# Kernel optimization log

Measured on AMD Instinct MI355X. Metric: run time of the kernel, lower is better.

## Reference

```python
import jax, jax.numpy as jnp
import numpy as np

N = 200000   # n+m+p+q
EMB = 32
K = 3
NNZ = 3200000


def _spmm(vals, rows, cols, X):
    # sparse [N,N] @ dense [N,EMB] via gather + segment-sum scatter
    return jax.ops.segment_sum(vals[:, None] * X[cols], rows, num_segments=N)


def setup_inputs() -> dict:
    key = jax.random.key(0)
    k1, k2, k3, k4 = jax.random.split(key, 4)
    A_vals = jax.random.uniform(k1, (NNZ,), dtype=jnp.float32)
    W0 = jax.random.normal(k2, (N, EMB), dtype=jnp.float32) * 0.01
    alpha = jnp.ones((K + 1,), dtype=jnp.float32) / (K + 1)
    A_rows = jax.random.randint(k3, (NNZ,), 0, N, dtype=jnp.int32)
    A_cols = jax.random.randint(k4, (NNZ,), 0, N, dtype=jnp.int32)
    return {"A_vals": A_vals, "W0": W0, "alpha": alpha,
            "A_rows": A_rows, "A_cols": A_cols}


def reference(A_vals, W0, alpha, A_rows, A_cols):
    E = _spmm(A_vals, A_rows, A_cols, W0)  # E0 = A @ W0
    a = jax.nn.softmax(alpha)
    E_final = a[0] * E
    for i in range(K):  # k-hop propagation, weighted accumulation fused
        E = _spmm(A_vals, A_rows, A_cols, E)
        E_final = E_final + a[i + 1] * E
    return E_final
```

## Files before the change

### kernel.cpp

```cpp
#include <hip/hip_runtime.h>

#define EMB 32
#define BSHIFT 10
#define RPB 1024
#define NB 256
#define TILE 4096
#define PT_THREADS 256
#define PT_ITEMS 16
#define SP_THREADS 1024
#define COLMASK 0x3FFFF


__global__ void bucket_hist_kernel(const int* __restrict__ rows, int nnz,
                                   int* __restrict__ bhist, int nb) {
    __shared__ int h[NB];
    int t = threadIdx.x;
    h[t] = 0;
    __syncthreads();
    int stride = gridDim.x * blockDim.x;
    for (int i = blockIdx.x * blockDim.x + t; i < nnz; i += stride)
        atomicAdd(&h[rows[i] >> BSHIFT], 1);
    __syncthreads();
    if (t < nb && h[t] > 0) atomicAdd(&bhist[t], h[t]);
}

__global__ __launch_bounds__(PT_THREADS) void partition_kernel(
        const float* __restrict__ vals, const int* __restrict__ rows,
        const int* __restrict__ cols, int nnz,
        const int* __restrict__ bhist, int* __restrict__ cursor,
        int2* __restrict__ pairs_stage, unsigned short* __restrict__ lrow_stage) {
    __shared__ int locbase[NB];
    __shared__ int h[NB];
    __shared__ int sc[NB];
    __shared__ int delta[NB];
    __shared__ float s_val[TILE];
    __shared__ int s_pack[TILE];
    __shared__ unsigned short s_bkt[TILE];
    const int t = threadIdx.x;
    const int tile_start = blockIdx.x * TILE;
    const int tile_cnt = min(TILE, nnz - tile_start);

    const int ownb = bhist[t];
    locbase[t] = ownb;
    h[t] = 0;
    __syncthreads();
    for (int off = 1; off < NB; off <<= 1) {
        int add = (t >= off) ? locbase[t - off] : 0;
        __syncthreads();
        locbase[t] += add;
        __syncthreads();
    }
    const int eb = locbase[t] - ownb;

    float v[PT_ITEMS];
    int pk[PT_ITEMS], b[PT_ITEMS];
    #pragma unroll
    for (int k = 0; k < PT_ITEMS; ++k) {
        int i = tile_start + t + k * PT_THREADS;
        if (i < nnz) {
            int r = rows[i];
            v[k] = vals[i];
            pk[k] = cols[i] | ((r & (RPB - 1)) << 18);
            b[k] = r >> BSHIFT;
            atomicAdd(&h[b[k]], 1);
        } else {
            b[k] = -1;
        }
    }
    __syncthreads();
    const int own = h[t];
    sc[t] = own;
    __syncthreads();
    for (int off = 1; off < NB; off <<= 1) {
        int add = (t >= off) ? sc[t - off] : 0;
        __syncthreads();
        sc[t] += add;
        __syncthreads();
    }
    const int excl = sc[t] - own;
    if (own > 0) {
        int old = atomicAdd(&cursor[t], own);
        delta[t] = (eb + old) - excl;
    }
    h[t] = excl;
    __syncthreads();
    #pragma unroll
    for (int k = 0; k < PT_ITEMS; ++k) {
        if (b[k] >= 0) {
            int rank = atomicAdd(&h[b[k]], 1);
            s_val[rank] = v[k];
            s_pack[rank] = pk[k];
            s_bkt[rank] = (unsigned short)b[k];
        }
    }
    __syncthreads();
    for (int i = t; i < tile_cnt; i += PT_THREADS) {
        int bb = s_bkt[i];
        int gpos = delta[bb] + i;
        int pk_i = s_pack[i];
        pairs_stage[gpos] = make_int2(__float_as_int(s_val[i]), pk_i);
        lrow_stage[gpos] = (unsigned short)(((unsigned)pk_i) >> 18);
    }
}

__global__ __launch_bounds__(SP_THREADS) void bucket_sort_kernel(
        const int2* __restrict__ pairs_stage, const unsigned short* __restrict__ lrow_stage,
        const int* __restrict__ bhist, int n, int nnz,
        int* __restrict__ row_ptr, int2* __restrict__ pairs) {
    __shared__ int rh[RPB];
    __shared__ int rc[RPB];
    const int bkt = blockIdx.x;
    const int t = threadIdx.x;

    if (t < NB) rh[t] = bhist[t];
    __syncthreads();
    for (int off = 1; off < NB; off <<= 1) {
        int add = 0;
        if (t < NB && t >= off) add = rh[t - off];
        __syncthreads();
        if (t < NB) rh[t] += add;
        __syncthreads();
    }
    const int i0 = (bkt > 0) ? rh[bkt - 1] : 0;
    const int i1 = rh[bkt];
    __syncthreads();

    const int row0 = bkt << BSHIFT;
    const int nrows = min(RPB, n - row0);
    rh[t] = 0;
    __syncthreads();
    for (int i = i0 + t; i < i1; i += SP_THREADS)
        atomicAdd(&rh[lrow_stage[i]], 1);
    __syncthreads();
    const int own = rh[t];
    for (int off = 1; off < SP_THREADS; off <<= 1) {
        int add = (t >= off) ? rh[t - off] : 0;
        __syncthreads();
        rh[t] += add;
        __syncthreads();
    }
    const int excl = rh[t] - own;
    if (t < nrows) row_ptr[row0 + t] = i0 + excl;
    rc[t] = excl;
    if (bkt == 0 && t == 0) row_ptr[n] = nnz;
    __syncthreads();
    for (int i = i0 + t; i < i1; i += SP_THREADS) {
        int2 p = pairs_stage[i];
        int r = lrow_stage[i];
        int pos = i0 + atomicAdd(&rc[r], 1);
        pairs[pos] = make_int2(p.x, p.y & COLMASK);
    }
}


__global__ void softmax4_kernel(const float* __restrict__ alpha, float* __restrict__ coefs) {
    if (threadIdx.x == 0 && blockIdx.x == 0) {
        float m = fmaxf(fmaxf(alpha[0], alpha[1]), fmaxf(alpha[2], alpha[3]));
        float e0 = __expf(alpha[0] - m), e1 = __expf(alpha[1] - m);
        float e2 = __expf(alpha[2] - m), e3 = __expf(alpha[3] - m);
        float inv = 1.0f / (e0 + e1 + e2 + e3);
        coefs[0] = e0 * inv; coefs[1] = e1 * inv; coefs[2] = e2 * inv; coefs[3] = e3 * inv;
    }
}


template <bool INIT, bool STORE_E>
__global__ __launch_bounds__(256) void spmm_kernel(
        const int* __restrict__ row_ptr, const int2* __restrict__ pairs,
        const float* __restrict__ X, float* __restrict__ Eout,
        float* __restrict__ Efin, const float* __restrict__ coefs,
        int hop, int n) {
    int tid = blockIdx.x * blockDim.x + threadIdx.x;
    int row = tid >> 3;
    if (row >= n) return;
    const int sub = (tid & 7) * 4;
    int j = row_ptr[row];
    const int j1 = row_ptr[row + 1];
    float ax = 0.f, ay = 0.f, az = 0.f, aw = 0.f;

    if ((j & 1) && j < j1) {
        int2 p = pairs[j];
        float v = __int_as_float(p.x);
        const float4 x = *reinterpret_cast<const float4*>(X + (size_t)p.y * EMB + sub);
        ax = fmaf(v, x.x, ax); ay = fmaf(v, x.y, ay);
        az = fmaf(v, x.z, az); aw = fmaf(v, x.w, aw);
        ++j;
    }
    for (; j + 4 <= j1; j += 4) {
        const int4 pa = *reinterpret_cast<const int4*>(pairs + j);
        const int4 pb = *reinterpret_cast<const int4*>(pairs + j + 2);
        const float4 x0 = *reinterpret_cast<const float4*>(X + (size_t)pa.y * EMB + sub);
        const float4 x1 = *reinterpret_cast<const float4*>(X + (size_t)pa.w * EMB + sub);
        const float4 x2 = *reinterpret_cast<const float4*>(X + (size_t)pb.y * EMB + sub);
        const float4 x3 = *reinterpret_cast<const float4*>(X + (size_t)pb.w * EMB + sub);
        const float v0 = __int_as_float(pa.x), v1 = __int_as_float(pa.z);
        const float v2 = __int_as_float(pb.x), v3 = __int_as_float(pb.z);
        ax = fmaf(v0, x0.x, ax); ay = fmaf(v0, x0.y, ay);
        az = fmaf(v0, x0.z, az); aw = fmaf(v0, x0.w, aw);
        ax = fmaf(v1, x1.x, ax); ay = fmaf(v1, x1.y, ay);
        az = fmaf(v1, x1.z, az); aw = fmaf(v1, x1.w, aw);
        ax = fmaf(v2, x2.x, ax); ay = fmaf(v2, x2.y, ay);
        az = fmaf(v2, x2.z, az); aw = fmaf(v2, x2.w, aw);
        ax = fmaf(v3, x3.x, ax); ay = fmaf(v3, x3.y, ay);
        az = fmaf(v3, x3.z, az); aw = fmaf(v3, x3.w, aw);
    }
    for (; j < j1; ++j) {
        int2 p = pairs[j];
        float v = __int_as_float(p.x);
        const float4 x = *reinterpret_cast<const float4*>(X + (size_t)p.y * EMB + sub);
        ax = fmaf(v, x.x, ax); ay = fmaf(v, x.y, ay);
        az = fmaf(v, x.z, az); aw = fmaf(v, x.w, aw);
    }

    const size_t o = (size_t)row * EMB + sub;
    if (STORE_E)
        *reinterpret_cast<float4*>(Eout + o) = make_float4(ax, ay, az, aw);
    const float a = coefs[hop];
    if (INIT) {
        *reinterpret_cast<float4*>(Efin + o) = make_float4(a * ax, a * ay, a * az, a * aw);
    } else {
        float4 f = *reinterpret_cast<const float4*>(Efin + o);
        f.x += a * ax; f.y += a * ay; f.z += a * az; f.w += a * aw;
        *reinterpret_cast<float4*>(Efin + o) = f;
    }
}


__global__ void spmm_atomic_kernel(const float* __restrict__ vals, const int* __restrict__ rows,
                                   const int* __restrict__ cols, int nnz,
                                   const float* __restrict__ X, float* __restrict__ Eout) {
    long long stride = (long long)gridDim.x * blockDim.x;
    long long total = (long long)nnz * 8;
    for (long long t = (long long)blockIdx.x * blockDim.x + threadIdx.x; t < total; t += stride) {
        int i = (int)(t >> 3);
        int sub = ((int)t & 7) * 4;
        float v = vals[i];
        const float4 x = *reinterpret_cast<const float4*>(X + (long long)cols[i] * EMB + sub);
        float* o = Eout + (long long)rows[i] * EMB + sub;
        atomicAdd(o + 0, v * x.x);
        atomicAdd(o + 1, v * x.y);
        atomicAdd(o + 2, v * x.z);
        atomicAdd(o + 3, v * x.w);
    }
}

template <bool INIT>
__global__ void axpy_kernel(const float* __restrict__ E, float* __restrict__ Efin,
                            const float* __restrict__ coefs, int hop, int total4) {
    int i = blockIdx.x * blockDim.x + threadIdx.x;
    if (i >= total4) return;
    float a = coefs[hop];
    float4 e = reinterpret_cast<const float4*>(E)[i];
    if (INIT) {
        reinterpret_cast<float4*>(Efin)[i] = make_float4(a * e.x, a * e.y, a * e.z, a * e.w);
    } else {
        float4 f = reinterpret_cast<float4*>(Efin)[i];
        f.x += a * e.x; f.y += a * e.y; f.z += a * e.z; f.w += a * e.w;
        reinterpret_cast<float4*>(Efin)[i] = f;
    }
}


extern "C" void kernel_launch(void* const* d_in, const int* in_sizes, int n_in,
                              void* d_out, int out_size, void* d_ws, size_t ws_size,
                              hipStream_t stream) {
    const float* A_vals = (const float*)d_in[0];
    const float* W0     = (const float*)d_in[1];
    const float* alpha  = (const float*)d_in[2];
    const int*   A_rows = (const int*)d_in[3];
    const int*   A_cols = (const int*)d_in[4];
    const int nnz = in_sizes[0];
    const int n   = in_sizes[1] / EMB;
    float* Efin = (float*)d_out;

    char* ws = (char*)d_ws;
    size_t off = 0;
    auto alloc = [&](size_t bytes) -> void* {
        void* p = (void*)(ws + off);
        off += (bytes + 255) & ~(size_t)255;
        return p;
    };

    float* Ebuf0 = (float*)alloc((size_t)n * EMB * 4);
    float* Ebuf1 = (float*)alloc((size_t)n * EMB * 4);
    float* coefs = (float*)alloc(4 * sizeof(float));
    int*  row_ptr = (int*)alloc((size_t)(n + 1) * 4);
    int*  bhist   = (int*)alloc(NB * 4);
    int*  cursor  = (int*)alloc(NB * 4);
    int2* pairs   = (int2*)alloc((size_t)nnz * 8);
    size_t off_csr = off;

    int2* pairs_stage = (int2*)Ebuf0;
    unsigned short* lrow_stage = (unsigned short*)Ebuf1;

    const int nb = (n + RPB - 1) >> BSHIFT;
    const bool use_csr = (ws_size >= off_csr) && (nb <= NB) && (n <= COLMASK + 1) &&
                         ((size_t)nnz * 8 <= (size_t)n * EMB * 4);

    softmax4_kernel<<<1, 64, 0, stream>>>(alpha, coefs);

    if (use_csr) {
        hipMemsetAsync(bhist, 0, 2 * NB * 4, stream);
        bucket_hist_kernel<<<1024, 256, 0, stream>>>(A_rows, nnz, bhist, nb);
        partition_kernel<<<(nnz + TILE - 1) / TILE, PT_THREADS, 0, stream>>>(
            A_vals, A_rows, A_cols, nnz, bhist, cursor, pairs_stage, lrow_stage);
        bucket_sort_kernel<<<nb, SP_THREADS, 0, stream>>>(
            pairs_stage, lrow_stage, bhist, n, nnz, row_ptr, pairs);

        int blocks = (n * 8 + 255) / 256;
        spmm_kernel<true,  true ><<<blocks, 256, 0, stream>>>(row_ptr, pairs, W0,    Ebuf0, Efin, coefs, 0, n);
        spmm_kernel<false, true ><<<blocks, 256, 0, stream>>>(row_ptr, pairs, Ebuf0, Ebuf1, Efin, coefs, 1, n);
        spmm_kernel<false, true ><<<blocks, 256, 0, stream>>>(row_ptr, pairs, Ebuf1, Ebuf0, Efin, coefs, 2, n);
        spmm_kernel<false, false><<<blocks, 256, 0, stream>>>(row_ptr, pairs, Ebuf0, Ebuf1, Efin, coefs, 3, n);
    } else {
        const float* X = W0;
        float* bufs[2] = {Ebuf0, Ebuf1};
        int total4 = n * EMB / 4;
        int ablocks = (total4 + 255) / 256;
        for (int hop = 0; hop < 4; ++hop) {
            float* Eo = bufs[hop & 1];
            hipMemsetAsync(Eo, 0, (size_t)n * EMB * 4, stream);
            spmm_atomic_kernel<<<2048, 256, 0, stream>>>(A_vals, A_rows, A_cols, nnz, X, Eo);
            if (hop == 0)
                axpy_kernel<true ><<<ablocks, 256, 0, stream>>>(Eo, Efin, coefs, hop, total4);
            else
                axpy_kernel<false><<<ablocks, 256, 0, stream>>>(Eo, Efin, coefs, hop, total4);
            X = Eo;
        }
    }
}
```

Before: 471.7 us.

## Bin rows by length within buckets and process two rows per thread group

The bucket sort now groups rows inside each 1024-row bucket by nonzero count and permutes them into slots. It emits a slot-ordered row pointer plus an order map back to the original rows, so neighbouring 8-lane groups in a wavefront get rows of similar length. The SpMM kernel then has each 8-lane group handle two adjacent slots at once, interleaving their gathers to raise memory-level parallelism. The aim is less load imbalance and divergence within wavefronts when row lengths are random. The cost is an extra indirection for output rows, scattered row writes, more registers per thread, and added work in the sort kernel.

```diff
diff --git a/kernel.cpp b/kernel.cpp
--- a/kernel.cpp
+++ b/kernel.cpp
@@ -105,18 +105,22 @@
 
 __global__ __launch_bounds__(SP_THREADS) void bucket_sort_kernel(
         const int2* __restrict__ pairs_stage, const unsigned short* __restrict__ lrow_stage,
-        const int* __restrict__ bhist, int n, int nnz,
-        int* __restrict__ row_ptr, int2* __restrict__ pairs) {
+        const int* __restrict__ bhist, int n, int nnz, int nb,
+        int* __restrict__ rps, int* __restrict__ order, int2* __restrict__ pairs) {
     __shared__ int rh[RPB];
+    __shared__ int pre[RPB];
     __shared__ int rc[RPB];
+    __shared__ unsigned short srOf[RPB];
+    __shared__ unsigned short tOf[RPB];
+    __shared__ int binCnt[66];
+    __shared__ int binBase[66];
     const int bkt = blockIdx.x;
     const int t = threadIdx.x;
 
     if (t < NB) rh[t] = bhist[t];
     __syncthreads();
     for (int off = 1; off < NB; off <<= 1) {
-        int add = 0;
-        if (t < NB && t >= off) add = rh[t - off];
+        int add = (t < NB && t >= off) ? rh[t - off] : 0;
         __syncthreads();
         if (t < NB) rh[t] += add;
         __syncthreads();
@@ -128,26 +132,46 @@
     const int row0 = bkt << BSHIFT;
     const int nrows = min(RPB, n - row0);
     rh[t] = 0;
+    if (t < 66) binCnt[t] = 0;
     __syncthreads();
     for (int i = i0 + t; i < i1; i += SP_THREADS)
         atomicAdd(&rh[lrow_stage[i]], 1);
     __syncthreads();
     const int own = rh[t];
-    for (int off = 1; off < SP_THREADS; off <<= 1) {
-        int add = (t >= off) ? rh[t - off] : 0;
-        __syncthreads();
-        rh[t] += add;
-        __syncthreads();
-    }
-    const int excl = rh[t] - own;
-    if (t < nrows) row_ptr[row0 + t] = i0 + excl;
-    rc[t] = excl;
-    if (bkt == 0 && t == 0) row_ptr[n] = nnz;
+    const bool valid = t < nrows;
+    const int bin = valid ? min(own, 63) : 65 - 1;
+    const int rb = atomicAdd(&binCnt[bin], 1);
+    __syncthreads();
+    if (t == 0) {
+        int s = 0;
+        for (int k = 0; k < 65; ++k) { binBase[k] = s; s += binCnt[k]; }
+    }
+    __syncthreads();
+    const int sr = binBase[bin] + rb;
+    srOf[t] = (unsigned short)sr;
+    tOf[sr] = (unsigned short)t;
+    pre[sr] = valid ? own : 0;
+    __syncthreads();
+    for (int off = 1; off < RPB; off <<= 1) {
+        int add = (t >= off) ? pre[t - off] : 0;
+        __syncthreads();
+        pre[t] += add;
+        __syncthreads();
+    }
+    const int tt = tOf[t];
+    const int lenSlot = rh[tt];
+    const int startSlot = pre[t] - lenSlot;
+    const int gslot = (bkt << BSHIFT) + t;
+    rps[gslot] = i0 + startSlot;
+    order[gslot] = (tt < nrows) ? (row0 + tt) : -1;
+    if (bkt == nb - 1 && t == 0) rps[nb << BSHIFT] = nnz;
+    __syncthreads();
+    rc[t] = i0 + (pre[srOf[t]] - rh[t]);
     __syncthreads();
     for (int i = i0 + t; i < i1; i += SP_THREADS) {
         int2 p = pairs_stage[i];
         int r = lrow_stage[i];
-        int pos = i0 + atomicAdd(&rc[r], 1);
+        int pos = atomicAdd(&rc[r], 1);
         pairs[pos] = make_int2(p.x, p.y & COLMASK);
     }
 }
@@ -166,27 +190,34 @@
 
 template <bool INIT, bool STORE_E>
 __global__ __launch_bounds__(256) void spmm_kernel(
-        const int* __restrict__ row_ptr, const int2* __restrict__ pairs,
-        const float* __restrict__ X, float* __restrict__ Eout,
-        float* __restrict__ Efin, const float* __restrict__ coefs,
-        int hop, int n) {
-    int tid = blockIdx.x * blockDim.x + threadIdx.x;
-    int row = tid >> 3;
-    if (row >= n) return;
+        const int* __restrict__ rps, const int* __restrict__ order,
+        const int2* __restrict__ pairs, const float* __restrict__ X,
+        float* __restrict__ Eout, float* __restrict__ Efin,
+        const float* __restrict__ coefs, int hop, int nslots) {
+    const int tid = blockIdx.x * blockDim.x + threadIdx.x;
+    const int g = tid >> 3;
+    const int slotA = g * 2, slotB = g * 2 + 1;
+    if (slotA >= nslots) return;
     const int sub = (tid & 7) * 4;
-    int j = row_ptr[row];
-    const int j1 = row_ptr[row + 1];
-    float ax = 0.f, ay = 0.f, az = 0.f, aw = 0.f;
-
-    if ((j & 1) && j < j1) {
+    int jA = rps[slotA];
+    const int eA = rps[slotA + 1];
+    const bool hasB = slotB < nslots;
+    int jB = hasB ? rps[slotB] : 0;
+    const int eB = hasB ? rps[slotB + 1] : 0;
+    const int rowA = order[slotA];
+    const int rowB = hasB ? order[slotB] : -1;
+
+    float aAx = 0.f, aAy = 0.f, aAz = 0.f, aAw = 0.f;
+    float aBx = 0.f, aBy = 0.f, aBz = 0.f, aBw = 0.f;
+
+    auto scal = [&](int j, float& x_, float& y_, float& z_, float& w_) {
         int2 p = pairs[j];
         float v = __int_as_float(p.x);
         const float4 x = *reinterpret_cast<const float4*>(X + (size_t)p.y * EMB + sub);
-        ax = fmaf(v, x.x, ax); ay = fmaf(v, x.y, ay);
-        az = fmaf(v, x.z, az); aw = fmaf(v, x.w, aw);
-        ++j;
-    }
-    for (; j + 4 <= j1; j += 4) {
+        x_ = fmaf(v, x.x, x_); y_ = fmaf(v, x.y, y_);
+        z_ = fmaf(v, x.z, z_); w_ = fmaf(v, x.w, w_);
+    };
+    auto quad = [&](int j, float& x_, float& y_, float& z_, float& w_) {
         const int4 pa = *reinterpret_cast<const int4*>(pairs + j);
         const int4 pb = *reinterpret_cast<const int4*>(pairs + j + 2);
         const float4 x0 = *reinterpret_cast<const float4*>(X + (size_t)pa.y * EMB + sub);
@@ -195,33 +226,84 @@
         const float4 x3 = *reinterpret_cast<const float4*>(X + (size_t)pb.w * EMB + sub);
         const float v0 = __int_as_float(pa.x), v1 = __int_as_float(pa.z);
         const float v2 = __int_as_float(pb.x), v3 = __int_as_float(pb.z);
-        ax = fmaf(v0, x0.x, ax); ay = fmaf(v0, x0.y, ay);
-        az = fmaf(v0, x0.z, az); aw = fmaf(v0, x0.w, aw);
-        ax = fmaf(v1, x1.x, ax); ay = fmaf(v1, x1.y, ay);
-        az = fmaf(v1, x1.z, az); aw = fmaf(v1, x1.w, aw);
-        ax = fmaf(v2, x2.x, ax); ay = fmaf(v2, x2.y, ay);
-        az = fmaf(v2, x2.z, az); aw = fmaf(v2, x2.w, aw);
-        ax = fmaf(v3, x3.x, ax); ay = fmaf(v3, x3.y, ay);
-        az = fmaf(v3, x3.z, az); aw = fmaf(v3, x3.w, aw);
-    }
-    for (; j < j1; ++j) {
-        int2 p = pairs[j];
-        float v = __int_as_float(p.x);
-        const float4 x = *reinterpret_cast<const float4*>(X + (size_t)p.y * EMB + sub);
-        ax = fmaf(v, x.x, ax); ay = fmaf(v, x.y, ay);
-        az = fmaf(v, x.z, az); aw = fmaf(v, x.w, aw);
-    }
-
-    const size_t o = (size_t)row * EMB + sub;
-    if (STORE_E)
-        *reinterpret_cast<float4*>(Eout + o) = make_float4(ax, ay, az, aw);
+        x_ = fmaf(v0, x0.x, x_); y_ = fmaf(v0, x0.y, y_);
+        z_ = fmaf(v0, x0.z, z_); w_ = fmaf(v0, x0.w, w_);
+        x_ = fmaf(v1, x1.x, x_); y_ = fmaf(v1, x1.y, y_);
+        z_ = fmaf(v1, x1.z, z_); w_ = fmaf(v1, x1.w, w_);
+        x_ = fmaf(v2, x2.x, x_); y_ = fmaf(v2, x2.y, y_);
+        z_ = fmaf(v2, x2.z, z_); w_ = fmaf(v2, x2.w, w_);
+        x_ = fmaf(v3, x3.x, x_); y_ = fmaf(v3, x3.y, y_);
+        z_ = fmaf(v3, x3.z, z_); w_ = fmaf(v3, x3.w, w_);
+    };
+
+    if ((jA & 1) && jA < eA) { scal(jA, aAx, aAy, aAz, aAw); ++jA; }
+    if ((jB & 1) && jB < eB) { scal(jB, aBx, aBy, aBz, aBw); ++jB; }
+
+    for (; jA + 4 <= eA && jB + 4 <= eB; jA += 4, jB += 4) {
+        const int4 pa0 = *reinterpret_cast<const int4*>(pairs + jA);
+        const int4 pa1 = *reinterpret_cast<const int4*>(pairs + jA + 2);
+        const int4 pb0 = *reinterpret_cast<const int4*>(pairs + jB);
+        const int4 pb1 = *reinterpret_cast<const int4*>(pairs + jB + 2);
+        const float4 xa0 = *reinterpret_cast<const float4*>(X + (size_t)pa0.y * EMB + sub);
+        const float4 xa1 = *reinterpret_cast<const float4*>(X + (size_t)pa0.w * EMB + sub);
+        const float4 xa2 = *reinterpret_cast<const float4*>(X + (size_t)pa1.y * EMB + sub);
+        const float4 xa3 = *reinterpret_cast<const float4*>(X + (size_t)pa1.w * EMB + sub);
+        const float4 xb0 = *reinterpret_cast<const float4*>(X + (size_t)pb0.y * EMB + sub);
+        const float4 xb1 = *reinterpret_cast<const float4*>(X + (size_t)pb0.w * EMB + sub);
+        const float4 xb2 = *reinterpret_cast<const float4*>(X + (size_t)pb1.y * EMB + sub);
+        const float4 xb3 = *reinterpret_cast<const float4*>(X + (size_t)pb1.w * EMB + sub);
+        const float va0 = __int_as_float(pa0.x), va1 = __int_as_float(pa0.z);
+        const float va2 = __int_as_float(pa1.x), va3 = __int_as_float(pa1.z);
+        const float vb0 = __int_as_float(pb0.x), vb1 = __int_as_float(pb0.z);
+        const float vb2 = __int_as_float(pb1.x), vb3 = __int_as_float(pb1.z);
+        aAx = fmaf(va0, xa0.x, aAx); aAy = fmaf(va0, xa0.y, aAy);
+        aAz = fmaf(va0, xa0.z, aAz); aAw = fmaf(va0, xa0.w, aAw);
+        aAx = fmaf(va1, xa1.x, aAx); aAy = fmaf(va1, xa1.y, aAy);
+        aAz = fmaf(va1, xa1.z, aAz); aAw = fmaf(va1, xa1.w, aAw);
+        aAx = fmaf(va2, xa2.x, aAx); aAy = fmaf(va2, xa2.y, aAy);
+        aAz = fmaf(va2, xa2.z, aAz); aAw = fmaf(va2, xa2.w, aAw);
+        aAx = fmaf(va3, xa3.x, aAx); aAy = fmaf(va3, xa3.y, aAy);
+        aAz = fmaf(va3, xa3.z, aAz); aAw = fmaf(va3, xa3.w, aAw);
+        aBx = fmaf(vb0, xb0.x, aBx); aBy = fmaf(vb0, xb0.y, aBy);
+        aBz = fmaf(vb0, xb0.z, aBz); aBw = fmaf(vb0, xb0.w, aBw);
+        aBx = fmaf(vb1, xb1.x, aBx); aBy = fmaf(vb1, xb1.y, aBy);
+        aBz = fmaf(vb1, xb1.z, aBz); aBw = fmaf(vb1, xb1.w, aBw);
+        aBx = fmaf(vb2, xb2.x, aBx); aBy = fmaf(vb2, xb2.y, aBy);
+        aBz = fmaf(vb2, xb2.z, aBz); aBw = fmaf(vb2, xb2.w, aBw);
+        aBx = fmaf(vb3, xb3.x, aBx); aBy = fmaf(vb3, xb3.y, aBy);
+        aBz = fmaf(vb3, xb3.z, aBz); aBw = fmaf(vb3, xb3.w, aBw);
+    }
+    for (; jA + 4 <= eA; jA += 4) quad(jA, aAx, aAy, aAz, aAw);
+    for (; jA < eA; ++jA) scal(jA, aAx, aAy, aAz, aAw);
+    for (; jB + 4 <= eB; jB += 4) quad(jB, aBx, aBy, aBz, aBw);
+    for (; jB < eB; ++jB) scal(jB, aBx, aBy, aBz, aBw);
+
     const float a = coefs[hop];
-    if (INIT) {
-        *reinterpret_cast<float4*>(Efin + o) = make_float4(a * ax, a * ay, a * az, a * aw);
-    } else {
-        float4 f = *reinterpret_cast<const float4*>(Efin + o);
-        f.x += a * ax; f.y += a * ay; f.z += a * az; f.w += a * aw;
-        *reinterpret_cast<float4*>(Efin + o) = f;
+    if (rowA >= 0) {
+        const size_t o = (size_t)rowA * EMB + sub;
+        if (STORE_E)
+            *reinterpret_cast<float4*>(Eout + o) = make_float4(aAx, aAy, aAz, aAw);
+        if (INIT) {
+            *reinterpret_cast<float4*>(Efin + o) =
+                make_float4(a * aAx, a * aAy, a * aAz, a * aAw);
+        } else {
+            float4 f = *reinterpret_cast<const float4*>(Efin + o);
+            f.x += a * aAx; f.y += a * aAy; f.z += a * aAz; f.w += a * aAw;
+            *reinterpret_cast<float4*>(Efin + o) = f;
+        }
+    }
+    if (rowB >= 0) {
+        const size_t o = (size_t)rowB * EMB + sub;
+        if (STORE_E)
+            *reinterpret_cast<float4*>(Eout + o) = make_float4(aBx, aBy, aBz, aBw);
+        if (INIT) {
+            *reinterpret_cast<float4*>(Efin + o) =
+                make_float4(a * aBx, a * aBy, a * aBz, a * aBw);
+        } else {
+            float4 f = *reinterpret_cast<const float4*>(Efin + o);
+            f.x += a * aBx; f.y += a * aBy; f.z += a * aBz; f.w += a * aBw;
+            *reinterpret_cast<float4*>(Efin + o) = f;
+        }
     }
 }
 
@@ -281,10 +363,14 @@
         return p;
     };
 
+    const int nb = (n + RPB - 1) >> BSHIFT;
+    const int nslots = nb << BSHIFT;
+
     float* Ebuf0 = (float*)alloc((size_t)n * EMB * 4);
     float* Ebuf1 = (float*)alloc((size_t)n * EMB * 4);
     float* coefs = (float*)alloc(4 * sizeof(float));
-    int*  row_ptr = (int*)alloc((size_t)(n + 1) * 4);
+    int*  rps     = (int*)alloc((size_t)(nslots + 1) * 4);
+    int*  order   = (int*)alloc((size_t)nslots * 4);
     int*  bhist   = (int*)alloc(NB * 4);
     int*  cursor  = (int*)alloc(NB * 4);
     int2* pairs   = (int2*)alloc((size_t)nnz * 8);
@@ -293,7 +379,6 @@
     int2* pairs_stage = (int2*)Ebuf0;
     unsigned short* lrow_stage = (unsigned short*)Ebuf1;
 
-    const int nb = (n + RPB - 1) >> BSHIFT;
     const bool use_csr = (ws_size >= off_csr) && (nb <= NB) && (n <= COLMASK + 1) &&
                          ((size_t)nnz * 8 <= (size_t)n * EMB * 4);
 
@@ -305,13 +390,14 @@
         partition_kernel<<<(nnz + TILE - 1) / TILE, PT_THREADS, 0, stream>>>(
             A_vals, A_rows, A_cols, nnz, bhist, cursor, pairs_stage, lrow_stage);
         bucket_sort_kernel<<<nb, SP_THREADS, 0, stream>>>(
-            pairs_stage, lrow_stage, bhist, n, nnz, row_ptr, pairs);
-
-        int blocks = (n * 8 + 255) / 256;
-        spmm_kernel<true,  true ><<<blocks, 256, 0, stream>>>(row_ptr, pairs, W0,    Ebuf0, Efin, coefs, 0, n);
-        spmm_kernel<false, true ><<<blocks, 256, 0, stream>>>(row_ptr, pairs, Ebuf0, Ebuf1, Efin, coefs, 1, n);
-        spmm_kernel<false, true ><<<blocks, 256, 0, stream>>>(row_ptr, pairs, Ebuf1, Ebuf0, Efin, coefs, 2, n);
-        spmm_kernel<false, false><<<blocks, 256, 0, stream>>>(row_ptr, pairs, Ebuf0, Ebuf1, Efin, coefs, 3, n);
+            pairs_stage, lrow_stage, bhist, n, nnz, nb, rps, order, pairs);
+
+        const int groups = (nslots + 1) / 2;
+        const int blocks = (groups * 8 + 255) / 256;
+        spmm_kernel<true,  true ><<<blocks, 256, 0, stream>>>(rps, order, pairs, W0,    Ebuf0, Efin, coefs, 0, nslots);
+        spmm_kernel<false, true ><<<blocks, 256, 0, stream>>>(rps, order, pairs, Ebuf0, Ebuf1, Efin, coefs, 1, nslots);
+        spmm_kernel<false, true ><<<blocks, 256, 0, stream>>>(rps, order, pairs, Ebuf1, Ebuf0, Efin, coefs, 2, nslots);
+        spmm_kernel<false, false><<<blocks, 256, 0, stream>>>(rps, order, pairs, Ebuf0, Ebuf1, Efin, coefs, 3, nslots);
     } else {
         const float* X = W0;
         float* bufs[2] = {Ebuf0, Ebuf1};
```

Measured after the change: 542.4 us. 1.15x slower.
